# Kernel tuning notes

Measured on AMD Instinct MI355X. Metric: run time of the kernel, lower is better.

Reference implementation:

```python
import math
import jax, jax.numpy as jnp
import numpy as np

B, S, DIM = 1, 2048, 2880
N_HEADS, N_KV, HD = 64, 8, 64
ROPE_FACTOR = 32.0
THETA = 150000.0
NEG_INF = -1e30


def setup_inputs() -> dict:
    key = jax.random.key(0)
    ks = jax.random.split(key, 12)
    std = 0.02
    x = jax.random.normal(ks[0], (B, S, DIM), jnp.float32)
    # rope cache: (S, 2*HD) = [cos | sin], rotate_half convention (angles duplicated)
    inv_freq = 1.0 / (THETA ** (np.arange(0, HD, 2, dtype=np.float32) / HD))
    angles = np.arange(S, dtype=np.float32)[:, None] * inv_freq[None, :]   # (S, HD/2)
    emb = np.concatenate([angles, angles], axis=-1)                        # (S, HD)
    rope_cache = jnp.asarray(np.concatenate([np.cos(emb), np.sin(emb)], axis=-1))  # (S, 2*HD)
    wq_w = jax.random.normal(ks[1], (N_HEADS * HD, DIM), jnp.float32) * std
    wq_b = jax.random.normal(ks[2], (N_HEADS * HD,), jnp.float32) * std
    wk_w = jax.random.normal(ks[3], (N_KV * HD, DIM), jnp.float32) * std
    wk_b = jax.random.normal(ks[4], (N_KV * HD,), jnp.float32) * std
    wv_w = jax.random.normal(ks[5], (N_KV * HD, DIM), jnp.float32) * std
    wv_b = jax.random.normal(ks[6], (N_KV * HD,), jnp.float32) * std
    wo_w = jax.random.normal(ks[7], (DIM, N_HEADS * HD), jnp.float32) * std
    wo_b = jax.random.normal(ks[8], (DIM,), jnp.float32) * std
    sinks = jax.random.normal(ks[9], (N_HEADS,), jnp.float32) * std
    return {"x": x, "rope_cache": rope_cache, "wq_w": wq_w, "wq_b": wq_b,
            "wk_w": wk_w, "wk_b": wk_b, "wv_w": wv_w, "wv_b": wv_b,
            "wo_w": wo_w, "wo_b": wo_b, "sinks": sinks, "sliding_window": 128}


def _rotate_half(t):
    t1, t2 = t[..., : HD // 2], t[..., HD // 2 :]
    return jnp.concatenate([-t2, t1], axis=-1)


def reference(x, rope_cache, wq_w, wq_b, wk_w, wk_b, wv_w, wv_b, wo_w, wo_b, sinks, sliding_window):
    bsz, seqlen, _ = x.shape
    mscale = 0.1 * math.log(ROPE_FACTOR) + 1.0
    scale = mscale / math.sqrt(HD)

    q = (x @ wq_w.T + wq_b).reshape(bsz, seqlen, N_HEADS, HD)
    k = (x @ wk_w.T + wk_b).reshape(bsz, seqlen, N_KV, HD)
    v = (x @ wv_w.T + wv_b).reshape(bsz, seqlen, N_KV, HD)

    cos = rope_cache[:seqlen, :HD][None, :, None, :]   # (1,S,1,HD)
    sin = rope_cache[:seqlen, HD:][None, :, None, :]
    q = q * cos + _rotate_half(q) * sin
    k = k * cos + _rotate_half(k) * sin

    q = q.transpose(0, 2, 1, 3)                        # (B,H,S,hd)
    n_rep = N_HEADS // N_KV
    k = jnp.repeat(k.transpose(0, 2, 1, 3), n_rep, axis=1)  # GQA expand
    v = jnp.repeat(v.transpose(0, 2, 1, 3), n_rep, axis=1)

    scores = jnp.einsum("bhqd,bhkd->bhqk", q, k) * scale
    i = jnp.arange(seqlen)[:, None]
    j = jnp.arange(seqlen)[None, :]
    mask = (j <= i) & ((i - j) < sliding_window)       # causal + sliding window
    scores = jnp.where(mask[None, None], scores, NEG_INF)

    lse = jax.nn.logsumexp(scores, axis=-1)            # (B,H,S)
    attn = jax.nn.softmax(scores, axis=-1)
    out = jnp.einsum("bhqk,bhkd->bhqd", attn, v)

    sink_scale = jax.nn.sigmoid(lse - sinks[None, :, None])[..., None]
    out = out * sink_scale

    out = out.transpose(0, 2, 1, 3).reshape(bsz, seqlen, N_HEADS * HD)
    return out @ wo_w.T + wo_b
```

## Files before the change

### kernel.cpp

```cpp
#include <hip/hip_runtime.h>
#include <hip/hip_bf16.h>
#include <math.h>
#include <stdint.h>


typedef __bf16 bf16x8 __attribute__((ext_vector_type(8)));
typedef float  f32x4  __attribute__((ext_vector_type(4)));
typedef uint32_t u32x4 __attribute__((ext_vector_type(4)));

#define MFMA_BF16(a,b,c) __builtin_amdgcn_mfma_f32_16x16x32_bf16((a),(b),(c),0,0,0)

#define XB   0L
#define WQB  5898240L
#define WKB  17694720L
#define WVB  19169280L
#define WOB  20643840L
#define QB   32440320L
#define KB   40828928L
#define VB   41877504L

__device__ __forceinline__ void gld_lds16(const void* g, void* l) {
    __builtin_amdgcn_global_load_lds(
        (__attribute__((address_space(1))) void*)(g),
        (__attribute__((address_space(3))) void*)(l), 16, 0, 0);
}

__device__ __forceinline__ bf16x8 ld8f(const float* p) {
    f32x4 a = *(const f32x4*)p;
    f32x4 b = *(const f32x4*)(p + 4);
    bf16x8 r;
#pragma unroll
    for (int t = 0; t < 4; t++) { r[t] = (__bf16)a[t]; r[t + 4] = (__bf16)b[t]; }
    return r;
}

__device__ __forceinline__ uint32_t pack2(float a, float b) {
    __bf16 x = (__bf16)a, y = (__bf16)b;
    return (uint32_t)__builtin_bit_cast(unsigned short, x)
         | ((uint32_t)__builtin_bit_cast(unsigned short, y) << 16);
}

__global__ __launch_bounds__(256) void convert_kernel(
    const float* __restrict__ x,  const float* __restrict__ wq,
    const float* __restrict__ wk, const float* __restrict__ wv,
    const float* __restrict__ wo, __bf16* __restrict__ dst)
{
    long e = ((long)blockIdx.x * 256 + threadIdx.x) * 8;
    const float* src; long off;
    if      (e <  WQB) { src = x;  off = e; }
    else if (e <  WKB) { src = wq; off = e - WQB; }
    else if (e <  WVB) { src = wk; off = e - WKB; }
    else if (e <  WOB) { src = wv; off = e - WVB; }
    else               { src = wo; off = e - WOB; }
    *(bf16x8*)(dst + e) = ld8f(src + off);
}

__device__ __forceinline__ void gemm_block64(
    const __bf16* __restrict__ A, const __bf16* __restrict__ W,
    const float* __restrict__ bias, __bf16* __restrict__ C,
    int N, int Ks, int kBeg, int kEnd, int m0, int n0,
    __bf16* As, __bf16* Bs)
{
    const int tid  = threadIdx.x;
    const int lane = tid & 63;
    const int wv   = tid >> 6;
    const int wm   = (wv >> 1) * 64;
    const int wn   = (wv & 1) * 64;
    const int quad = lane >> 4;
    const int c    = lane & 15;

    const int srow = tid >> 2;
    const int scol = (tid & 3) * 8;

    int br0 = n0 + srow;      if (br0 > N - 1) br0 = N - 1;
    int br1 = n0 + 64 + srow; if (br1 > N - 1) br1 = N - 1;
    const __bf16* pa0 = A + (size_t)(m0 + srow) * Ks + scol;
    const __bf16* pa1 = A + (size_t)(m0 + 64 + srow) * Ks + scol;
    const __bf16* pb0 = W + (size_t)br0 * Ks + scol;
    const __bf16* pb1 = W + (size_t)br1 * Ks + scol;

    f32x4 acc[4][4];
#pragma unroll
    for (int i = 0; i < 4; i++)
#pragma unroll
        for (int j = 0; j < 4; j++) acc[i][j] = (f32x4){0.f, 0.f, 0.f, 0.f};

    for (int kk = kBeg; kk < kEnd; kk += 64) {
        gld_lds16(pa0 + kk,      As + tid * 8);
        gld_lds16(pa1 + kk,      As + 2048 + tid * 8);
        gld_lds16(pa0 + kk + 32, As + 4096 + tid * 8);
        gld_lds16(pa1 + kk + 32, As + 6144 + tid * 8);
        gld_lds16(pb0 + kk,      Bs + tid * 8);
        gld_lds16(pb1 + kk,      Bs + 2048 + tid * 8);
        gld_lds16(pb0 + kk + 32, Bs + 4096 + tid * 8);
        gld_lds16(pb1 + kk + 32, Bs + 6144 + tid * 8);
        __syncthreads();
        for (int kt = 0; kt < 2; kt++) {
            bf16x8 af[4], bfv[4];
#pragma unroll
            for (int i = 0; i < 4; i++)
                af[i] = *(const bf16x8*)&As[kt * 4096 + (wm + i * 16 + c) * 32 + quad * 8];
#pragma unroll
            for (int j = 0; j < 4; j++)
                bfv[j] = *(const bf16x8*)&Bs[kt * 4096 + (wn + j * 16 + c) * 32 + quad * 8];
#pragma unroll
            for (int i = 0; i < 4; i++)
#pragma unroll
                for (int j = 0; j < 4; j++)
                    acc[i][j] = MFMA_BF16(af[i], bfv[j], acc[i][j]);
        }
        __syncthreads();
    }

#pragma unroll
    for (int j = 0; j < 4; j++) {
        int col = n0 + wn + j * 16 + c;
        if (col >= N) continue;
        float bv = bias ? bias[col] : 0.0f;
#pragma unroll
        for (int i = 0; i < 4; i++) {
            int row = m0 + wm + i * 16 + quad * 4;
#pragma unroll
            for (int r = 0; r < 4; r++)
                C[(size_t)(row + r) * N + col] = (__bf16)(acc[i][j][r] + bv);
        }
    }
}

__global__ __launch_bounds__(256, 3) void qkv_kernel(
    const __bf16* __restrict__ x,
    const __bf16* __restrict__ wq, const float* __restrict__ bq,
    const __bf16* __restrict__ wk, const float* __restrict__ bk,
    const __bf16* __restrict__ wv, const float* __restrict__ bv,
    __bf16* __restrict__ qo, __bf16* __restrict__ ko, __bf16* __restrict__ vo)
{
    __shared__ __align__(16) __bf16 As[8192], Bs[8192];
    const int by = blockIdx.y;
    const __bf16 *W; const float* bias; __bf16* C; int N, n0;
    if (by < 32)      { W = wq; bias = bq; C = qo; N = 4096; n0 = by * 128; }
    else if (by < 36) { W = wk; bias = bk; C = ko; N = 512;  n0 = (by - 32) * 128; }
    else              { W = wv; bias = bv; C = vo; N = 512;  n0 = (by - 36) * 128; }
    gemm_block64(x, W, bias, C, N, 2880, 0, 2880, blockIdx.x * 128, n0, As, Bs);
}

__global__ __launch_bounds__(256, 3) void oproj_kernel(
    const __bf16* __restrict__ a, const __bf16* __restrict__ w,
    __bf16* __restrict__ p0, __bf16* __restrict__ p1)
{
    __shared__ __align__(16) __bf16 As[8192], Bs[8192];
    const int z = blockIdx.z;
    __bf16* C = z ? p1 : p0;
    gemm_block64(a, w, nullptr, C, 2880, 4096, z * 2048, (z + 1) * 2048,
                 blockIdx.x * 128, blockIdx.y * 128, As, Bs);
}

__global__ __launch_bounds__(256) void reduce_kernel(
    const __bf16* __restrict__ p0, const __bf16* __restrict__ p1,
    const float* __restrict__ bo, float* __restrict__ out)
{
    long e = ((long)blockIdx.x * 256 + threadIdx.x) * 8;
    int col = (int)(e % 2880L);
    bf16x8 a = *(const bf16x8*)(p0 + e);
    bf16x8 b = *(const bf16x8*)(p1 + e);
    f32x4 o0, o1;
#pragma unroll
    for (int t = 0; t < 4; t++) {
        o0[t] = (float)a[t]     + (float)b[t]     + bo[col + t];
        o1[t] = (float)a[4 + t] + (float)b[4 + t] + bo[col + 4 + t];
    }
    *(f32x4*)(out + e)     = o0;
    *(f32x4*)(out + e + 4) = o1;
}

__global__ __launch_bounds__(512) void attn_kernel(
    __bf16* __restrict__ q, const __bf16* __restrict__ k,
    const __bf16* __restrict__ v, const float* __restrict__ sinks,
    const float* __restrict__ rope)
{
    __shared__ __align__(16) __bf16 Ks[192 * 72];
    __shared__ __align__(16) __bf16 Vt[64 * 200];

    const int tid = threadIdx.x, lane = tid & 63, w = tid >> 6;
    const int quad = lane >> 4, c = lane & 15;
    const int i0  = blockIdx.x * 64;
    const int kvh = blockIdx.y;
    const int h   = kvh * 8 + w;
    const int k0  = i0 - 128;
    const float scale = 0.16832169878499658f;

#pragma unroll
    for (int it = 0; it < 2; it++) {
        int unit = it * 512 + tid;
        if (unit < 768) {
            int krow = unit >> 2;
            int kdg  = (unit & 3) * 8;
            int j = k0 + krow; if (j < 0) j = 0;
            const __bf16* gp = k + (size_t)j * 512 + kvh * 64 + kdg;
            bf16x8 x1 = *(const bf16x8*)(gp);
            bf16x8 x2 = *(const bf16x8*)(gp + 32);
            const float* rc = rope + (size_t)j * 128 + kdg;
            bf16x8 o1, o2;
#pragma unroll
            for (int t = 0; t < 8; t++) {
                float cc = rc[t], si = rc[64 + t];
                float a = (float)x1[t], b = (float)x2[t];
                o1[t] = (__bf16)(a * cc - b * si);
                o2[t] = (__bf16)(b * cc + a * si);
            }
            *(bf16x8*)&Ks[krow * 72 + kdg]      = o1;
            *(bf16x8*)&Ks[krow * 72 + kdg + 32] = o2;
        }
    }

    {
        const int vrow = tid & 63;
        const int d0   = (tid >> 6) * 8;
#pragma unroll
        for (int it = 0; it < 3; it++) {
            int s = it * 64 + vrow;
            int j = k0 + s; if (j < 0) j = 0;
            bf16x8 t = *(const bf16x8*)(v + (size_t)j * 512 + kvh * 64 + d0);
#pragma unroll
            for (int u = 0; u < 8; u++) Vt[(d0 + u) * 200 + s] = t[u];
        }
    }

    bf16x8 qf[4][2];
#pragma unroll
    for (int f = 0; f < 4; f++) {
        const int row = i0 + f * 16 + c;
        const __bf16* gp = q + (size_t)row * 4096 + h * 64 + quad * 8;
        bf16x8 x1 = *(const bf16x8*)(gp);
        bf16x8 x2 = *(const bf16x8*)(gp + 32);
        const float* rc = rope + (size_t)row * 128 + quad * 8;
        bf16x8 o1, o2;
#pragma unroll
        for (int t = 0; t < 8; t++) {
            float cc = rc[t] * scale, si = rc[64 + t] * scale;
            float a = (float)x1[t], b = (float)x2[t];
            o1[t] = (__bf16)(a * cc - b * si);
            o2[t] = (__bf16)(b * cc + a * si);
        }
        qf[f][0] = o1; qf[f][1] = o2;
    }

    __syncthreads();

    const float sk   = sinks[h];
    const int laneA  = ((quad & 1) << 5) + c;
    const int laneB  = laneA + 16;
    const bool hiSel = (quad >> 1) != 0;
    const int db     = 128 + c - quad * 4;

#pragma unroll
    for (int f = 0; f < 4; f++) {
        f32x4 acc9[9];
#pragma unroll
        for (int jj = 0; jj < 9; jj++) acc9[jj] = (f32x4){0.f, 0.f, 0.f, 0.f};
        __builtin_amdgcn_s_setprio(1);
#pragma unroll
        for (int jj = 0; jj < 9; jj++) {
            const int j = f + jj;
#pragma unroll
            for (int kt = 0; kt < 2; kt++) {
                bf16x8 kf = *(const bf16x8*)&Ks[(j * 16 + c) * 72 + kt * 32 + quad * 8];
                acc9[jj] = MFMA_BF16(kf, qf[f][kt], acc9[jj]);
            }
        }
        __builtin_amdgcn_s_setprio(0);

        const int jgb = k0 + f * 16 + quad * 4;
        float rmax = -3.0e4f;
#pragma unroll
        for (int jj = 0; jj < 9; jj++)
#pragma unroll
            for (int r = 0; r < 4; r++) {
                int d  = db  - jj * 16 - r;
                int jg = jgb + jj * 16 + r;
                bool ok = ((unsigned)d < 128u) && (jg >= 0);
                float vv = ok ? acc9[jj][r] : -3.0e4f;
                acc9[jj][r] = vv;
                rmax = fmaxf(rmax, vv);
            }
        rmax = fmaxf(rmax, __shfl_xor(rmax, 16));
        rmax = fmaxf(rmax, __shfl_xor(rmax, 32));

        float rs = 0.f;
#pragma unroll
        for (int jj = 0; jj < 9; jj++)
#pragma unroll
            for (int r = 0; r < 4; r++) {
                float e = __expf(acc9[jj][r] - rmax);
                acc9[jj][r] = e;
                rs += e;
            }
        rs += __shfl_xor(rs, 16);
        rs += __shfl_xor(rs, 32);

        float s   = fmaxf(rs, 1e-20f);
        float lse = rmax + __logf(s);
        float fac = 1.f / ((1.f + __expf(sk - lse)) * s);

        uint32_t pk[24];
#pragma unroll
        for (int t = 0; t < 24; t++) pk[t] = 0;
#pragma unroll
        for (int jj = 0; jj < 9; jj++) {
            const int j = f + jj;
            pk[2 * j]     = pack2(acc9[jj][0] * fac, acc9[jj][1] * fac);
            pk[2 * j + 1] = pack2(acc9[jj][2] * fac, acc9[jj][3] * fac);
        }

        f32x4 acc2[4];
#pragma unroll
        for (int jd = 0; jd < 4; jd++) acc2[jd] = (f32x4){0.f, 0.f, 0.f, 0.f};
        const int kt0 = f >> 1;
#pragma unroll
        for (int kk = 0; kk < 5; kk++) {
            const int kt = kt0 + kk;
            uint32_t l0  = (uint32_t)__shfl((int)pk[4 * kt],     laneA);
            uint32_t h0  = (uint32_t)__shfl((int)pk[4 * kt + 1], laneA);
            uint32_t l0b = (uint32_t)__shfl((int)pk[4 * kt],     laneB);
            uint32_t h0b = (uint32_t)__shfl((int)pk[4 * kt + 1], laneB);
            uint32_t l1  = (uint32_t)__shfl((int)pk[4 * kt + 2], laneA);
            uint32_t h1  = (uint32_t)__shfl((int)pk[4 * kt + 3], laneA);
            uint32_t l1b = (uint32_t)__shfl((int)pk[4 * kt + 2], laneB);
            uint32_t h1b = (uint32_t)__shfl((int)pk[4 * kt + 3], laneB);
            u32x4 wv = { hiSel ? l1  : l0,  hiSel ? h1  : h0,
                         hiSel ? l1b : l0b, hiSel ? h1b : h0b };
            bf16x8 pa = __builtin_bit_cast(bf16x8, wv);
            __builtin_amdgcn_s_setprio(1);
#pragma unroll
            for (int jd = 0; jd < 4; jd++) {
                bf16x8 bv = *(const bf16x8*)&Vt[(jd * 16 + c) * 200 + kt * 32 + quad * 8];
                acc2[jd] = MFMA_BF16(pa, bv, acc2[jd]);
            }
            __builtin_amdgcn_s_setprio(0);
        }

#pragma unroll
        for (int jd = 0; jd < 4; jd++)
#pragma unroll
            for (int r = 0; r < 4; r++)
                q[(size_t)(i0 + f * 16 + quad * 4 + r) * 4096 + h * 64 + jd * 16 + c]
                    = (__bf16)acc2[jd][r];
    }
}

extern "C" void kernel_launch(void* const* d_in, const int* in_sizes, int n_in,
                              void* d_out, int out_size, void* d_ws, size_t ws_size,
                              hipStream_t stream) {
    const float* x    = (const float*)d_in[0];
    const float* rope = (const float*)d_in[1];
    const float* wq   = (const float*)d_in[2];
    const float* bq   = (const float*)d_in[3];
    const float* wk   = (const float*)d_in[4];
    const float* bk   = (const float*)d_in[5];
    const float* wv   = (const float*)d_in[6];
    const float* bv   = (const float*)d_in[7];
    const float* wo   = (const float*)d_in[8];
    const float* bo   = (const float*)d_in[9];
    const float* sk   = (const float*)d_in[10];
    float* out = (float*)d_out;

    __bf16* wsb = (__bf16*)d_ws;
    __bf16* xb  = wsb + XB;
    __bf16* wqb = wsb + WQB;
    __bf16* wkb = wsb + WKB;
    __bf16* wvb = wsb + WVB;
    __bf16* wob = wsb + WOB;
    __bf16* qb  = wsb + QB;
    __bf16* kb  = wsb + KB;
    __bf16* vb  = wsb + VB;
    __bf16* po0 = wsb + 0L;
    __bf16* po1 = wsb + 5898240L;

    convert_kernel<<<15840, 256, 0, stream>>>(x, wq, wk, wv, wo, xb);
    qkv_kernel<<<dim3(16, 40), 256, 0, stream>>>(xb, wqb, bq, wkb, bk, wvb, bv,
                                                 qb, kb, vb);
    attn_kernel<<<dim3(32, 8), 512, 0, stream>>>(qb, kb, vb, sk, rope);
    oproj_kernel<<<dim3(16, 23, 2), 256, 0, stream>>>(qb, wob, po0, po1);
    reduce_kernel<<<2880, 256, 0, stream>>>(po0, po1, bo, out);
}
```

Before: 332.6 us.

## Remap GEMM workgroups across XCDs and template attention f-steps to shrink registers

The QKV and output-projection GEMM kernels remap the linear block id so that consecutive workgroups dispatched round-robin across the 8 XCDs land on contiguous tiles, aiming for better L2 reuse of shared A/B panels per XCD. The attention inner loop over four query sub-tiles is split into a templated per-step function with a smaller packed-probability array (20 instead of 24 entries), relative indexing, and interleaved K-fragment loads, intended to cut register pressure and dynamic indexing. The remap relies on the grid sizes (640 and 368 blocks) being divisible by 8; otherwise it would produce wrong tiles.

```diff
diff --git a/kernel.cpp b/kernel.cpp
--- a/kernel.cpp
+++ b/kernel.cpp
@@ -135,12 +135,15 @@
     __bf16* __restrict__ qo, __bf16* __restrict__ ko, __bf16* __restrict__ vo)
 {
     __shared__ __align__(16) __bf16 As[8192], Bs[8192];
-    const int by = blockIdx.y;
+    const int orig = blockIdx.y * 16 + blockIdx.x;
+    const int wg   = (orig & 7) * 80 + (orig >> 3);
+    const int bx   = wg & 15;
+    const int by   = wg >> 4;
     const __bf16 *W; const float* bias; __bf16* C; int N, n0;
     if (by < 32)      { W = wq; bias = bq; C = qo; N = 4096; n0 = by * 128; }
     else if (by < 36) { W = wk; bias = bk; C = ko; N = 512;  n0 = (by - 32) * 128; }
     else              { W = wv; bias = bv; C = vo; N = 512;  n0 = (by - 36) * 128; }
-    gemm_block64(x, W, bias, C, N, 2880, 0, 2880, blockIdx.x * 128, n0, As, Bs);
+    gemm_block64(x, W, bias, C, N, 2880, 0, 2880, bx * 128, n0, As, Bs);
 }
 
 __global__ __launch_bounds__(256, 3) void oproj_kernel(
@@ -150,8 +153,12 @@
     __shared__ __align__(16) __bf16 As[8192], Bs[8192];
     const int z = blockIdx.z;
     __bf16* C = z ? p1 : p0;
+    const int orig = blockIdx.y * 16 + blockIdx.x;
+    const int wg   = (orig & 7) * 46 + (orig >> 3);
+    const int bx   = wg & 15;
+    const int by   = wg >> 4;
     gemm_block64(a, w, nullptr, C, 2880, 4096, z * 2048, (z + 1) * 2048,
-                 blockIdx.x * 128, blockIdx.y * 128, As, Bs);
+                 bx * 128, by * 128, As, Bs);
 }
 
 __global__ __launch_bounds__(256) void reduce_kernel(
@@ -170,6 +177,103 @@
     }
     *(f32x4*)(out + e)     = o0;
     *(f32x4*)(out + e + 4) = o1;
+}
+
+template<int F>
+__device__ __forceinline__ void attn_f_step(
+    const __bf16* __restrict__ Ks, const __bf16* __restrict__ Vt,
+    __bf16* __restrict__ q, bf16x8 qf0, bf16x8 qf1,
+    int i0, int h, int k0, float sk,
+    int c, int quad, int laneA, int laneB, bool hiSel, int db)
+{
+    f32x4 acc9[9];
+#pragma unroll
+    for (int jj = 0; jj < 9; jj++) acc9[jj] = (f32x4){0.f, 0.f, 0.f, 0.f};
+    __builtin_amdgcn_s_setprio(1);
+#pragma unroll
+    for (int jj = 0; jj < 9; jj++) {
+        const int j = F + jj;
+        bf16x8 kf0 = *(const bf16x8*)&Ks[(j * 16 + c) * 72 + quad * 8];
+        bf16x8 kf1 = *(const bf16x8*)&Ks[(j * 16 + c) * 72 + 32 + quad * 8];
+        acc9[jj] = MFMA_BF16(kf0, qf0, acc9[jj]);
+        acc9[jj] = MFMA_BF16(kf1, qf1, acc9[jj]);
+    }
+    __builtin_amdgcn_s_setprio(0);
+
+    const int jgb = k0 + F * 16 + quad * 4;
+    float rmax = -3.0e4f;
+#pragma unroll
+    for (int jj = 0; jj < 9; jj++)
+#pragma unroll
+        for (int r = 0; r < 4; r++) {
+            int d  = db  - jj * 16 - r;
+            int jg = jgb + jj * 16 + r;
+            bool ok = ((unsigned)d < 128u) && (jg >= 0);
+            float vv = ok ? acc9[jj][r] : -3.0e4f;
+            acc9[jj][r] = vv;
+            rmax = fmaxf(rmax, vv);
+        }
+    rmax = fmaxf(rmax, __shfl_xor(rmax, 16));
+    rmax = fmaxf(rmax, __shfl_xor(rmax, 32));
+
+    float rs = 0.f;
+#pragma unroll
+    for (int jj = 0; jj < 9; jj++)
+#pragma unroll
+        for (int r = 0; r < 4; r++) {
+            float e = __expf(acc9[jj][r] - rmax);
+            acc9[jj][r] = e;
+            rs += e;
+        }
+    rs += __shfl_xor(rs, 16);
+    rs += __shfl_xor(rs, 32);
+
+    float s   = fmaxf(rs, 1e-20f);
+    float lse = rmax + __logf(s);
+    float fac = 1.f / ((1.f + __expf(sk - lse)) * s);
+
+    uint32_t pk[20];
+#pragma unroll
+    for (int t = 0; t < 20; t++) pk[t] = 0;
+#pragma unroll
+    for (int jj = 0; jj < 9; jj++) {
+        const int li = (F & 1) ? (2 * jj + 2) : (2 * jj);
+        pk[li]     = pack2(acc9[jj][0] * fac, acc9[jj][1] * fac);
+        pk[li + 1] = pack2(acc9[jj][2] * fac, acc9[jj][3] * fac);
+    }
+
+    f32x4 acc2[4];
+#pragma unroll
+    for (int jd = 0; jd < 4; jd++) acc2[jd] = (f32x4){0.f, 0.f, 0.f, 0.f};
+#pragma unroll
+    for (int kk = 0; kk < 5; kk++) {
+        const int kt = (F >> 1) + kk;
+        uint32_t l0  = (uint32_t)__shfl((int)pk[4 * kk],     laneA);
+        uint32_t h0  = (uint32_t)__shfl((int)pk[4 * kk + 1], laneA);
+        uint32_t l0b = (uint32_t)__shfl((int)pk[4 * kk],     laneB);
+        uint32_t h0b = (uint32_t)__shfl((int)pk[4 * kk + 1], laneB);
+        uint32_t l1  = (uint32_t)__shfl((int)pk[4 * kk + 2], laneA);
+        uint32_t h1  = (uint32_t)__shfl((int)pk[4 * kk + 3], laneA);
+        uint32_t l1b = (uint32_t)__shfl((int)pk[4 * kk + 2], laneB);
+        uint32_t h1b = (uint32_t)__shfl((int)pk[4 * kk + 3], laneB);
+        u32x4 wvv = { hiSel ? l1  : l0,  hiSel ? h1  : h0,
+                      hiSel ? l1b : l0b, hiSel ? h1b : h0b };
+        bf16x8 pa = __builtin_bit_cast(bf16x8, wvv);
+        __builtin_amdgcn_s_setprio(1);
+#pragma unroll
+        for (int jd = 0; jd < 4; jd++) {
+            bf16x8 bv = *(const bf16x8*)&Vt[(jd * 16 + c) * 200 + kt * 32 + quad * 8];
+            acc2[jd] = MFMA_BF16(pa, bv, acc2[jd]);
+        }
+        __builtin_amdgcn_s_setprio(0);
+    }
+
+#pragma unroll
+    for (int jd = 0; jd < 4; jd++)
+#pragma unroll
+        for (int r = 0; r < 4; r++)
+            q[(size_t)(i0 + F * 16 + quad * 4 + r) * 4096 + h * 64 + jd * 16 + c]
+                = (__bf16)acc2[jd][r];
 }
 
 __global__ __launch_bounds__(512) void attn_kernel(
@@ -252,99 +356,10 @@
     const bool hiSel = (quad >> 1) != 0;
     const int db     = 128 + c - quad * 4;
 
-#pragma unroll
-    for (int f = 0; f < 4; f++) {
-        f32x4 acc9[9];
-#pragma unroll
-        for (int jj = 0; jj < 9; jj++) acc9[jj] = (f32x4){0.f, 0.f, 0.f, 0.f};
-        __builtin_amdgcn_s_setprio(1);
-#pragma unroll
-        for (int jj = 0; jj < 9; jj++) {
-            const int j = f + jj;
-#pragma unroll
-            for (int kt = 0; kt < 2; kt++) {
-                bf16x8 kf = *(const bf16x8*)&Ks[(j * 16 + c) * 72 + kt * 32 + quad * 8];
-                acc9[jj] = MFMA_BF16(kf, qf[f][kt], acc9[jj]);
-            }
-        }
-        __builtin_amdgcn_s_setprio(0);
-
-        const int jgb = k0 + f * 16 + quad * 4;
-        float rmax = -3.0e4f;
-#pragma unroll
-        for (int jj = 0; jj < 9; jj++)
-#pragma unroll
-            for (int r = 0; r < 4; r++) {
-                int d  = db  - jj * 16 - r;
-                int jg = jgb + jj * 16 + r;
-                bool ok = ((unsigned)d < 128u) && (jg >= 0);
-                float vv = ok ? acc9[jj][r] : -3.0e4f;
-                acc9[jj][r] = vv;
-                rmax = fmaxf(rmax, vv);
-            }
-        rmax = fmaxf(rmax, __shfl_xor(rmax, 16));
-        rmax = fmaxf(rmax, __shfl_xor(rmax, 32));
-
-        float rs = 0.f;
-#pragma unroll
-        for (int jj = 0; jj < 9; jj++)
-#pragma unroll
-            for (int r = 0; r < 4; r++) {
-                float e = __expf(acc9[jj][r] - rmax);
-                acc9[jj][r] = e;
-                rs += e;
-            }
-        rs += __shfl_xor(rs, 16);
-        rs += __shfl_xor(rs, 32);
-
-        float s   = fmaxf(rs, 1e-20f);
-        float lse = rmax + __logf(s);
-        float fac = 1.f / ((1.f + __expf(sk - lse)) * s);
-
-        uint32_t pk[24];
-#pragma unroll
-        for (int t = 0; t < 24; t++) pk[t] = 0;
-#pragma unroll
-        for (int jj = 0; jj < 9; jj++) {
-            const int j = f + jj;
-            pk[2 * j]     = pack2(acc9[jj][0] * fac, acc9[jj][1] * fac);
-            pk[2 * j + 1] = pack2(acc9[jj][2] * fac, acc9[jj][3] * fac);
-        }
-
-        f32x4 acc2[4];
-#pragma unroll
-        for (int jd = 0; jd < 4; jd++) acc2[jd] = (f32x4){0.f, 0.f, 0.f, 0.f};
-        const int kt0 = f >> 1;
-#pragma unroll
-        for (int kk = 0; kk < 5; kk++) {
-            const int kt = kt0 + kk;
-            uint32_t l0  = (uint32_t)__shfl((int)pk[4 * kt],     laneA);
-            uint32_t h0  = (uint32_t)__shfl((int)pk[4 * kt + 1], laneA);
-            uint32_t l0b = (uint32_t)__shfl((int)pk[4 * kt],     laneB);
-            uint32_t h0b = (uint32_t)__shfl((int)pk[4 * kt + 1], laneB);
-            uint32_t l1  = (uint32_t)__shfl((int)pk[4 * kt + 2], laneA);
-            uint32_t h1  = (uint32_t)__shfl((int)pk[4 * kt + 3], laneA);
-            uint32_t l1b = (uint32_t)__shfl((int)pk[4 * kt + 2], laneB);
-            uint32_t h1b = (uint32_t)__shfl((int)pk[4 * kt + 3], laneB);
-            u32x4 wv = { hiSel ? l1  : l0,  hiSel ? h1  : h0,
-                         hiSel ? l1b : l0b, hiSel ? h1b : h0b };
-            bf16x8 pa = __builtin_bit_cast(bf16x8, wv);
-            __builtin_amdgcn_s_setprio(1);
-#pragma unroll
-            for (int jd = 0; jd < 4; jd++) {
-                bf16x8 bv = *(const bf16x8*)&Vt[(jd * 16 + c) * 200 + kt * 32 + quad * 8];
-                acc2[jd] = MFMA_BF16(pa, bv, acc2[jd]);
-            }
-            __builtin_amdgcn_s_setprio(0);
-        }
-
-#pragma unroll
-        for (int jd = 0; jd < 4; jd++)
-#pragma unroll
-            for (int r = 0; r < 4; r++)
-                q[(size_t)(i0 + f * 16 + quad * 4 + r) * 4096 + h * 64 + jd * 16 + c]
-                    = (__bf16)acc2[jd][r];
-    }
+    attn_f_step<0>(Ks, Vt, q, qf[0][0], qf[0][1], i0, h, k0, sk, c, quad, laneA, laneB, hiSel, db);
+    attn_f_step<1>(Ks, Vt, q, qf[1][0], qf[1][1], i0, h, k0, sk, c, quad, laneA, laneB, hiSel, db);
+    attn_f_step<2>(Ks, Vt, q, qf[2][0], qf[2][1], i0, h, k0, sk, c, quad, laneA, laneB, hiSel, db);
+    attn_f_step<3>(Ks, Vt, q, qf[3][0], qf[3][1], i0, h, k0, sk, c, quad, laneA, laneB, hiSel, db);
 }
 
 extern "C" void kernel_launch(void* const* d_in, const int* in_sizes, int n_in,
```

New measurement: 330.1 us. Within noise of the previous version (-0.8%).
